# Kernel optimization log

Hardware: AMD Instinct MI355X
Metric: run time of the kernel (lower is better)

## Reference

```python
import jax, jax.numpy as jnp
import numpy as np

B, S, D = 4, 2048, 1024


def setup_inputs() -> dict:
    key = jax.random.key(0)
    ks = jax.random.split(key, 7)
    s = 1.0 / np.sqrt(D)
    return {
        "x": jax.random.normal(ks[0], (B, S, D), dtype=jnp.float32),
        "Wq": jax.random.normal(ks[1], (D, D), dtype=jnp.float32) * s,
        "bq": jax.random.normal(ks[2], (D,), dtype=jnp.float32) * s,
        "Wk": jax.random.normal(ks[3], (D, D), dtype=jnp.float32) * s,
        "bk": jax.random.normal(ks[4], (D,), dtype=jnp.float32) * s,
        "Wv": jax.random.normal(ks[5], (D, D), dtype=jnp.float32) * s,
        "bv": jax.random.normal(ks[6], (D,), dtype=jnp.float32) * s,
    }


def reference(x, Wq, bq, Wk, bk, Wv, bv):
    # Linear layers: y = x @ W^T + b (torch nn.Linear convention)
    Q = jnp.einsum("bsd,ed->bse", x, Wq) + bq  # [B,S,D]
    K = jnp.einsum("bsd,ed->bse", x, Wk) + bk
    V = jnp.einsum("bsd,ed->bse", x, Wv) + bv
    d = x.shape[-1]
    scores = jnp.einsum("bqd,bkd->bqk", Q, K) / jnp.sqrt(jnp.float32(d))  # [B,S,S]
    weights = jax.nn.softmax(scores, axis=-1)
    O = jnp.einsum("bqk,bkd->bqd", weights, V)  # [B,S,D]
    return O
```

## Files before the change

kernel.cpp:

```cpp
#include <hip/hip_runtime.h>

typedef __bf16    bf16x8 __attribute__((ext_vector_type(8)));
typedef __bf16    bf16x4 __attribute__((ext_vector_type(4)));
typedef float     f32x4  __attribute__((ext_vector_type(4)));

#define BM 128
#define BN 128
#define BK 64

__device__ __forceinline__ void gload_lds16(const __bf16* g, __bf16* l) {
  __builtin_amdgcn_global_load_lds(
      (const __attribute__((address_space(1))) void*)g,
      (__attribute__((address_space(3))) void*)l,
      16, 0, 0);
}

__global__ void cvt_all(const float* __restrict__ x, const float* __restrict__ Wq,
                        const float* __restrict__ Wk, const float* __restrict__ Wv,
                        __bf16* __restrict__ xb, __bf16* __restrict__ Wqk,
                        __bf16* __restrict__ Wvb, float* __restrict__ lsum) {
  int b = blockIdx.x;
  if (b == 0) {
    for (int j = threadIdx.x; j < 8192; j += 256) lsum[j] = 0.f;
  }
  const float* src;
  __bf16* dst;
  int i;
  if (b < 8192) {
    src = x; dst = xb; i = b * 256 + threadIdx.x;
  } else {
    b -= 8192;
    const int mat = b >> 10;
    i = (b & 1023) * 256 + threadIdx.x;
    src = (mat == 0) ? Wq : (mat == 1) ? Wk : Wv;
    dst = (mat == 0) ? Wqk : (mat == 1) ? (Wqk + 1048576) : Wvb;
  }
  float4 v = ((const float4*)src)[i];
  bf16x4 o;
  o[0] = (__bf16)v.x; o[1] = (__bf16)v.y; o[2] = (__bf16)v.z; o[3] = (__bf16)v.w;
  ((bf16x4*)dst)[i] = o;
}

template<int MODE>
__global__ __launch_bounds__(256, 2)
void gemm_bt(const __bf16* __restrict__ A, const __bf16* __restrict__ B,
             float* __restrict__ C,
             int lda, int ldb, int ldc, int K,
             long sA, long sB, long sC,
             const float* __restrict__ bias0, const float* __restrict__ bias1,
             float* __restrict__ lsum,
             __bf16* __restrict__ out0, __bf16* __restrict__ out1)
{
  A += (long)blockIdx.z * sA;
  B += (long)blockIdx.z * sB;

  const int tid  = threadIdx.x;
  const int wave = tid >> 6;
  const int lane = tid & 63;
  const int quad = lane >> 4;
  const int l15  = lane & 15;
  const int bm0  = blockIdx.x * BM;
  const int bn0  = blockIdx.y * BN;
  const int wm   = (wave >> 1) * 64;
  const int wn   = (wave & 1) * 64;

  __shared__ __align__(16) __bf16 As[BM * BK];
  __shared__ __align__(16) __bf16 Bs[BN * BK];

  f32x4 acc[4][4];
#pragma unroll
  for (int i = 0; i < 4; ++i)
#pragma unroll
    for (int j = 0; j < 4; ++j)
      acc[i][j] = (f32x4){0.f, 0.f, 0.f, 0.f};

  const __bf16* Ag[4];
  const __bf16* Bg[4];
#pragma unroll
  for (int c = 0; c < 4; ++c) {
    const int r  = c * 32 + (tid >> 3);
    const int g  = (tid & 7) ^ (r & 7);
    Ag[c] = A + (size_t)(bm0 + r) * lda + g * 8;
    Bg[c] = B + (size_t)(bn0 + r) * ldb + g * 8;
  }

  for (int k0 = 0; k0 < K; k0 += BK) {
#pragma unroll
    for (int c = 0; c < 4; ++c) {
      gload_lds16(Ag[c] + k0, &As[c * 2048 + tid * 8]);
      gload_lds16(Bg[c] + k0, &Bs[c * 2048 + tid * 8]);
    }
    __syncthreads();

#pragma unroll
    for (int kk = 0; kk < 2; ++kk) {
      bf16x8 af[4], bfv[4];
#pragma unroll
      for (int i = 0; i < 4; ++i) {
        const int R = wm + i * 16 + l15;
        af[i] = *(const bf16x8*)&As[R * BK + (((kk * 4 + quad) ^ (R & 7)) * 8)];
      }
#pragma unroll
      for (int i = 0; i < 4; ++i) {
        const int R = wn + i * 16 + l15;
        bfv[i] = *(const bf16x8*)&Bs[R * BK + (((kk * 4 + quad) ^ (R & 7)) * 8)];
      }
#pragma unroll
      for (int mi = 0; mi < 4; ++mi)
#pragma unroll
        for (int ni = 0; ni < 4; ++ni)
          acc[mi][ni] = __builtin_amdgcn_mfma_f32_16x16x32_bf16(
              af[mi], bfv[ni], acc[mi][ni], 0, 0, 0);
    }
    __syncthreads();
  }

  if (MODE == 2) {
#pragma unroll
    for (int mi = 0; mi < 4; ++mi) {
#pragma unroll
      for (int r = 0; r < 4; ++r) {
        const int gm = bm0 + wm + mi * 16 + quad * 4 + r;
        float part = 0.f;
#pragma unroll
        for (int ni = 0; ni < 4; ++ni) {
          const int gn = bn0 + wn + ni * 16 + l15;
          const __bf16 eb = (__bf16)__expf(acc[mi][ni][r] * 0.03125f);
          out0[(long)blockIdx.z * sC + (size_t)gm * ldc + gn] = eb;
          part += (float)eb;
        }
        part += __shfl_xor(part, 1);
        part += __shfl_xor(part, 2);
        part += __shfl_xor(part, 4);
        part += __shfl_xor(part, 8);
        if (l15 == 0)
          atomicAdd(&lsum[blockIdx.z * 2048 + gm], part);
      }
    }
  } else if (MODE == 3) {
#pragma unroll
    for (int mi = 0; mi < 4; ++mi) {
#pragma unroll
      for (int r = 0; r < 4; ++r) {
        const int gm = bm0 + wm + mi * 16 + quad * 4 + r;
        const float rv = 1.0f / lsum[blockIdx.z * 2048 + gm];
#pragma unroll
        for (int ni = 0; ni < 4; ++ni) {
          const int gn = bn0 + wn + ni * 16 + l15;
          C[(long)blockIdx.z * sC + (size_t)gm * ldc + gn] = acc[mi][ni][r] * rv;
        }
      }
    }
  } else {
#pragma unroll
    for (int mi = 0; mi < 4; ++mi) {
#pragma unroll
      for (int ni = 0; ni < 4; ++ni) {
        const int gn = bn0 + wn + ni * 16 + l15;
#pragma unroll
        for (int r = 0; r < 4; ++r) {
          const int gm = bm0 + wm + mi * 16 + quad * 4 + r;
          float v = acc[mi][ni][r];
          if (MODE == 0) {
            const int mat = gn >> 10;
            const int d   = gn & 1023;
            const float* bias = (mat == 0) ? bias0 : bias1;
            __bf16* dst = (mat == 0) ? out0 : out1;
            dst[(size_t)gm * 1024 + d] = (__bf16)(v + bias[d]);
          } else {
            const int b = gn >> 11, s = gn & 2047;
            out0[(size_t)b * (1024 * 2048) + (size_t)gm * 2048 + s] =
                (__bf16)(v + bias0[gm]);
          }
        }
      }
    }
  }
}

extern "C" void kernel_launch(void* const* d_in, const int* in_sizes, int n_in,
                              void* d_out, int out_size, void* d_ws, size_t ws_size,
                              hipStream_t stream) {
  const float* x  = (const float*)d_in[0];
  const float* Wq = (const float*)d_in[1];
  const float* bq = (const float*)d_in[2];
  const float* Wk = (const float*)d_in[3];
  const float* bk = (const float*)d_in[4];
  const float* Wv = (const float*)d_in[5];
  const float* bv = (const float*)d_in[6];
  float* out = (float*)d_out;

  char* ws = (char*)d_ws;
  __bf16* Q    = (__bf16*)(ws);
  __bf16* Kb   = (__bf16*)(ws + (16ull << 20));
  __bf16* Vt   = (__bf16*)(ws + (32ull << 20));
  __bf16* xb   = (__bf16*)(ws + (48ull << 20));
  __bf16* Wqk  = (__bf16*)(ws + (64ull << 20));
  __bf16* Wvb  = (__bf16*)(ws + (68ull << 20));
  __bf16* Sc   = (__bf16*)(ws + (48ull << 20));
  float*  lsum = (float*)(ws + (110ull << 20));

  dim3 blk(256);

  cvt_all<<<11264, blk, 0, stream>>>(x, Wq, Wk, Wv, xb, Wqk, Wvb, lsum);

  gemm_bt<0><<<dim3(64, 16, 1), blk, 0, stream>>>(
      xb, Wqk, nullptr, 1024, 1024, 0, 1024,
      0L, 0L, 0L, bq, bk, nullptr, Q, Kb);

  gemm_bt<1><<<dim3(8, 64, 1), blk, 0, stream>>>(
      Wvb, xb, nullptr, 1024, 1024, 0, 1024,
      0L, 0L, 0L, bv, nullptr, nullptr, Vt, nullptr);

  gemm_bt<2><<<dim3(16, 16, 4), blk, 0, stream>>>(
      Q, Kb, nullptr, 1024, 1024, 2048, 1024,
      2048L * 1024, 2048L * 1024, 2048L * 2048,
      nullptr, nullptr, lsum, Sc, nullptr);

  gemm_bt<3><<<dim3(16, 8, 4), blk, 0, stream>>>(
      Sc, Vt, out, 2048, 2048, 1024, 2048,
      2048L * 2048, 1024L * 2048, 2048L * 1024,
      nullptr, nullptr, lsum, nullptr, nullptr);
}
```

Before: 235.9 us.

## Fuse V projection into QKV GEMM with LDS-transposed V output and BK=128

Merges the separate V projection GEMM into the Q/K projection launch by concatenating Wq, Wk and Wv into one weight buffer and widening the grid. Blocks that produce V stage their tile in LDS with a swizzle and write it transposed with 16-byte vector stores, instead of the old scattered per-element transposed writes. The K tile depth is also raised from 64 to 128 for all GEMMs, which halves the number of barriers per K loop. The cost is double the shared memory per block, which may lower occupancy, and an extra LDS pass in the V epilogue.

New measurement: 237.3 us. No clear change (+0.6%).

```diff
diff --git a/kernel.cpp b/kernel.cpp
--- a/kernel.cpp
+++ b/kernel.cpp
@@ -6,7 +6,6 @@
 
 #define BM 128
 #define BN 128
-#define BK 64
 
 __device__ __forceinline__ void gload_lds16(const __bf16* g, __bf16* l) {
   __builtin_amdgcn_global_load_lds(
@@ -17,8 +16,8 @@
 
 __global__ void cvt_all(const float* __restrict__ x, const float* __restrict__ Wq,
                         const float* __restrict__ Wk, const float* __restrict__ Wv,
-                        __bf16* __restrict__ xb, __bf16* __restrict__ Wqk,
-                        __bf16* __restrict__ Wvb, float* __restrict__ lsum) {
+                        __bf16* __restrict__ xb, __bf16* __restrict__ Wqkv,
+                        float* __restrict__ lsum) {
   int b = blockIdx.x;
   if (b == 0) {
     for (int j = threadIdx.x; j < 8192; j += 256) lsum[j] = 0.f;
@@ -33,7 +32,7 @@
     const int mat = b >> 10;
     i = (b & 1023) * 256 + threadIdx.x;
     src = (mat == 0) ? Wq : (mat == 1) ? Wk : Wv;
-    dst = (mat == 0) ? Wqk : (mat == 1) ? (Wqk + 1048576) : Wvb;
+    dst = Wqkv + (size_t)mat * 1048576;
   }
   float4 v = ((const float4*)src)[i];
   bf16x4 o;
@@ -41,16 +40,21 @@
   ((bf16x4*)dst)[i] = o;
 }
 
-template<int MODE>
+template<int MODE, int BKT>
 __global__ __launch_bounds__(256, 2)
 void gemm_bt(const __bf16* __restrict__ A, const __bf16* __restrict__ B,
              float* __restrict__ C,
              int lda, int ldb, int ldc, int K,
              long sA, long sB, long sC,
-             const float* __restrict__ bias0, const float* __restrict__ bias1,
-             float* __restrict__ lsum,
-             __bf16* __restrict__ out0, __bf16* __restrict__ out1)
+             const float* __restrict__ bq, const float* __restrict__ bk,
+             const float* __restrict__ bv, float* __restrict__ lsum,
+             __bf16* __restrict__ out0, __bf16* __restrict__ out1,
+             __bf16* __restrict__ out2)
 {
+  constexpr int NCH = (BM * BKT) / (256 * 8);
+  constexpr int GPR = BKT / 8;
+  constexpr int RPC = 2048 / BKT;
+
   A += (long)blockIdx.z * sA;
   B += (long)blockIdx.z * sB;
 
@@ -64,8 +68,8 @@
   const int wm   = (wave >> 1) * 64;
   const int wn   = (wave & 1) * 64;
 
-  __shared__ __align__(16) __bf16 As[BM * BK];
-  __shared__ __align__(16) __bf16 Bs[BN * BK];
+  __shared__ __align__(16) __bf16 As[BM * BKT];
+  __shared__ __align__(16) __bf16 Bs[BN * BKT];
 
   f32x4 acc[4][4];
 #pragma unroll
@@ -74,36 +78,36 @@
     for (int j = 0; j < 4; ++j)
       acc[i][j] = (f32x4){0.f, 0.f, 0.f, 0.f};
 
-  const __bf16* Ag[4];
-  const __bf16* Bg[4];
-#pragma unroll
-  for (int c = 0; c < 4; ++c) {
-    const int r  = c * 32 + (tid >> 3);
-    const int g  = (tid & 7) ^ (r & 7);
+  const __bf16* Ag[NCH];
+  const __bf16* Bg[NCH];
+#pragma unroll
+  for (int c = 0; c < NCH; ++c) {
+    const int r = c * RPC + tid / GPR;
+    const int g = (tid & (GPR - 1)) ^ (r & 7);
     Ag[c] = A + (size_t)(bm0 + r) * lda + g * 8;
     Bg[c] = B + (size_t)(bn0 + r) * ldb + g * 8;
   }
 
-  for (int k0 = 0; k0 < K; k0 += BK) {
-#pragma unroll
-    for (int c = 0; c < 4; ++c) {
+  for (int k0 = 0; k0 < K; k0 += BKT) {
+#pragma unroll
+    for (int c = 0; c < NCH; ++c) {
       gload_lds16(Ag[c] + k0, &As[c * 2048 + tid * 8]);
       gload_lds16(Bg[c] + k0, &Bs[c * 2048 + tid * 8]);
     }
     __syncthreads();
 
 #pragma unroll
-    for (int kk = 0; kk < 2; ++kk) {
+    for (int kk = 0; kk < BKT / 32; ++kk) {
       bf16x8 af[4], bfv[4];
 #pragma unroll
       for (int i = 0; i < 4; ++i) {
         const int R = wm + i * 16 + l15;
-        af[i] = *(const bf16x8*)&As[R * BK + (((kk * 4 + quad) ^ (R & 7)) * 8)];
+        af[i] = *(const bf16x8*)&As[R * BKT + (((kk * 4 + quad) ^ (R & 7)) * 8)];
       }
 #pragma unroll
       for (int i = 0; i < 4; ++i) {
         const int R = wn + i * 16 + l15;
-        bfv[i] = *(const bf16x8*)&Bs[R * BK + (((kk * 4 + quad) ^ (R & 7)) * 8)];
+        bfv[i] = *(const bf16x8*)&Bs[R * BKT + (((kk * 4 + quad) ^ (R & 7)) * 8)];
       }
 #pragma unroll
       for (int mi = 0; mi < 4; ++mi)
@@ -115,7 +119,55 @@
     __syncthreads();
   }
 
-  if (MODE == 2) {
+  if (MODE == 0 && bn0 >= 2048) {
+    __bf16* LT = As;
+    const int d0 = bn0 - 2048;
+#pragma unroll
+    for (int mi = 0; mi < 4; ++mi) {
+      const int mb   = wm + mi * 16 + quad * 4;
+      const int Gw   = mb >> 3;
+      const int moff = mb & 7;
+#pragma unroll
+      for (int ni = 0; ni < 4; ++ni) {
+        const int dl = wn + ni * 16 + l15;
+        const float bias = bv[d0 + dl];
+        bf16x4 tv;
+#pragma unroll
+        for (int r = 0; r < 4; ++r)
+          tv[r] = (__bf16)(acc[mi][ni][r] + bias);
+        *(bf16x4*)&LT[dl * 128 + ((Gw ^ (dl & 15)) * 8) + moff] = tv;
+      }
+    }
+    __syncthreads();
+    const int bI = bm0 >> 11;
+    const int s0 = bm0 & 2047;
+#pragma unroll
+    for (int j = 0; j < 8; ++j) {
+      const int idx = j * 2048 + tid * 8;
+      const int dl  = idx >> 7;
+      const int sl  = idx & 127;
+      const int sg  = sl >> 3;
+      bf16x8 v = *(const bf16x8*)&LT[dl * 128 + ((sg ^ (dl & 15)) * 8)];
+      *(bf16x8*)&out2[((size_t)bI * 1024 + d0 + dl) * 2048 + s0 + sl] = v;
+    }
+  } else if (MODE == 0) {
+#pragma unroll
+    for (int mi = 0; mi < 4; ++mi) {
+#pragma unroll
+      for (int ni = 0; ni < 4; ++ni) {
+        const int gn  = bn0 + wn + ni * 16 + l15;
+        const int mat = gn >> 10;
+        const int d   = gn & 1023;
+        const float bias = (mat == 0) ? bq[d] : bk[d];
+        __bf16* dst = (mat == 0) ? out0 : out1;
+#pragma unroll
+        for (int r = 0; r < 4; ++r) {
+          const int gm = bm0 + wm + mi * 16 + quad * 4 + r;
+          dst[(size_t)gm * 1024 + d] = (__bf16)(acc[mi][ni][r] + bias);
+        }
+      }
+    }
+  } else if (MODE == 2) {
 #pragma unroll
     for (int mi = 0; mi < 4; ++mi) {
 #pragma unroll
@@ -137,7 +189,7 @@
           atomicAdd(&lsum[blockIdx.z * 2048 + gm], part);
       }
     }
-  } else if (MODE == 3) {
+  } else {
 #pragma unroll
     for (int mi = 0; mi < 4; ++mi) {
 #pragma unroll
@@ -148,30 +200,6 @@
         for (int ni = 0; ni < 4; ++ni) {
           const int gn = bn0 + wn + ni * 16 + l15;
           C[(long)blockIdx.z * sC + (size_t)gm * ldc + gn] = acc[mi][ni][r] * rv;
-        }
-      }
-    }
-  } else {
-#pragma unroll
-    for (int mi = 0; mi < 4; ++mi) {
-#pragma unroll
-      for (int ni = 0; ni < 4; ++ni) {
-        const int gn = bn0 + wn + ni * 16 + l15;
-#pragma unroll
-        for (int r = 0; r < 4; ++r) {
-          const int gm = bm0 + wm + mi * 16 + quad * 4 + r;
-          float v = acc[mi][ni][r];
-          if (MODE == 0) {
-            const int mat = gn >> 10;
-            const int d   = gn & 1023;
-            const float* bias = (mat == 0) ? bias0 : bias1;
-            __bf16* dst = (mat == 0) ? out0 : out1;
-            dst[(size_t)gm * 1024 + d] = (__bf16)(v + bias[d]);
-          } else {
-            const int b = gn >> 11, s = gn & 2047;
-            out0[(size_t)b * (1024 * 2048) + (size_t)gm * 2048 + s] =
-                (__bf16)(v + bias0[gm]);
-          }
         }
       }
     }
@@ -195,30 +223,25 @@
   __bf16* Kb   = (__bf16*)(ws + (16ull << 20));
   __bf16* Vt   = (__bf16*)(ws + (32ull << 20));
   __bf16* xb   = (__bf16*)(ws + (48ull << 20));
-  __bf16* Wqk  = (__bf16*)(ws + (64ull << 20));
-  __bf16* Wvb  = (__bf16*)(ws + (68ull << 20));
+  __bf16* Wqkv = (__bf16*)(ws + (64ull << 20));
   __bf16* Sc   = (__bf16*)(ws + (48ull << 20));
   float*  lsum = (float*)(ws + (110ull << 20));
 
   dim3 blk(256);
 
-  cvt_all<<<11264, blk, 0, stream>>>(x, Wq, Wk, Wv, xb, Wqk, Wvb, lsum);
-
-  gemm_bt<0><<<dim3(64, 16, 1), blk, 0, stream>>>(
-      xb, Wqk, nullptr, 1024, 1024, 0, 1024,
-      0L, 0L, 0L, bq, bk, nullptr, Q, Kb);
-
-  gemm_bt<1><<<dim3(8, 64, 1), blk, 0, stream>>>(
-      Wvb, xb, nullptr, 1024, 1024, 0, 1024,
-      0L, 0L, 0L, bv, nullptr, nullptr, Vt, nullptr);
-
-  gemm_bt<2><<<dim3(16, 16, 4), blk, 0, stream>>>(
+  cvt_all<<<11264, blk, 0, stream>>>(x, Wq, Wk, Wv, xb, Wqkv, lsum);
+
+  gemm_bt<0, 128><<<dim3(64, 24, 1), blk, 0, stream>>>(
+      xb, Wqkv, nullptr, 1024, 1024, 0, 1024,
+      0L, 0L, 0L, bq, bk, bv, nullptr, Q, Kb, Vt);
+
+  gemm_bt<2, 128><<<dim3(16, 16, 4), blk, 0, stream>>>(
       Q, Kb, nullptr, 1024, 1024, 2048, 1024,
       2048L * 1024, 2048L * 1024, 2048L * 2048,
-      nullptr, nullptr, lsum, Sc, nullptr);
-
-  gemm_bt<3><<<dim3(16, 8, 4), blk, 0, stream>>>(
+      nullptr, nullptr, nullptr, lsum, Sc, nullptr, nullptr);
+
+  gemm_bt<3, 128><<<dim3(16, 8, 4), blk, 0, stream>>>(
       Sc, Vt, out, 2048, 2048, 1024, 2048,
       2048L * 2048, 1024L * 2048, 2048L * 1024,
-      nullptr, nullptr, lsum, nullptr, nullptr);
-}
+      nullptr, nullptr, nullptr, lsum, nullptr, nullptr, nullptr);
+}
```
